# Kernel tuning notes

Measured on AMD Instinct MI355X. Metric: run time of the kernel, lower is better.

Reference implementation:

```python
import jax, jax.numpy as jnp
import numpy as np

B, S, D, H = 2, 2048, 1024, 16
DK = D // H

def setup_inputs() -> dict:
    key = jax.random.key(0)
    ks = jax.random.split(key, 12)
    def lin(k, shape, fan_in):
        bound = 1.0 / np.sqrt(fan_in)
        return jax.random.uniform(k, shape, jnp.float32, -bound, bound)
    inp = {
        'Q': jax.random.normal(ks[0], (B, S, D), jnp.float32),
        'K': jax.random.normal(ks[1], (B, S, D), jnp.float32),
        'V': jax.random.normal(ks[2], (B, S, D), jnp.float32),
        # padding mask: last 128 key positions of batch element 0 are padding
        'padding_mask': jnp.ones((B, 1, 1, S), jnp.int32).at[0, :, :, -128:].set(0),
        # causal look-ahead mask
        'look_ahead_mask': jnp.tril(jnp.ones((S, S), jnp.int32))[None, None],
        'Wq': lin(ks[3], (D, D), D), 'bq': lin(ks[4], (D,), D),
        'Wk': lin(ks[5], (D, D), D), 'bk': lin(ks[6], (D,), D),
        'Wv': lin(ks[7], (D, D), D), 'bv': lin(ks[8], (D,), D),
        'Wo': lin(ks[9], (D, D), D), 'bo': lin(ks[10], (D,), D),
    }
    return inp

def _split_heads(x):
    # [B,S,D] -> [B,H,S,DK]
    b, s, _ = x.shape
    return x.reshape(b, s, H, DK).transpose(0, 2, 1, 3)

def reference(Q, K, V, padding_mask, look_ahead_mask, Wq, bq, Wk, bk, Wv, bv, Wo, bo):
    q = _split_heads(Q @ Wq.T + bq)  # [B,H,S,DK]
    k = _split_heads(K @ Wk.T + bk)
    v = _split_heads(V @ Wv.T + bv)
    scores = jnp.einsum('bhqd,bhkd->bhqk', q, k) / np.sqrt(DK).astype(np.float32)
    neg_inf = jnp.float32(-jnp.inf)
    scores = jnp.where(padding_mask == 0, neg_inf, scores)
    scores = jnp.where(look_ahead_mask == 0, neg_inf, scores)
    weights = jax.nn.softmax(scores, axis=-1)  # dropout is identity in eval mode
    x = jnp.einsum('bhqk,bhkd->bhqd', weights, v)  # [B,H,S,DK]
    x = x.transpose(0, 2, 1, 3).reshape(Q.shape[0], Q.shape[1], D)
    return x @ Wo.T + bo
```

## Files before the change

kernel.cpp:

```cpp
#include <hip/hip_runtime.h>
#include <hip/hip_bf16.h>

#define B_   2
#define S_   2048
#define D_   1024
#define H_   16
#define DK_  64

typedef unsigned short u16;
typedef __attribute__((ext_vector_type(8))) short bf16x8;
typedef __attribute__((ext_vector_type(4))) float f32x4;

#define CHUNK_   12
#define NSLOT_   48

static __device__ __forceinline__ u16 f2bf(float f) {
  union { float f; unsigned u; } v; v.f = f;
  unsigned r = v.u + 0x7FFF + ((v.u >> 16) & 1);
  return (u16)(r >> 16);
}

static __device__ __forceinline__ void gl_lds16(const void* g, void* l) {
  __builtin_amdgcn_global_load_lds(
      (const __attribute__((address_space(1))) void*)g,
      (__attribute__((address_space(3))) void*)l, 16, 0, 0);
}

__global__ void cvt7(const float4* __restrict__ i0, const float4* __restrict__ i1,
                     const float4* __restrict__ i2, const float4* __restrict__ i3,
                     const float4* __restrict__ i4, const float4* __restrict__ i5,
                     const float4* __restrict__ i6,
                     ushort4* __restrict__ o0, ushort4* __restrict__ o1,
                     ushort4* __restrict__ o2, ushort4* __restrict__ o3,
                     ushort4* __restrict__ o4, ushort4* __restrict__ o5,
                     ushort4* __restrict__ o6, int nbig, int nsmall) {
  int y = blockIdx.y;
  const float4* in; ushort4* out; int bound;
  switch (y) {
    case 0: in = i0; out = o0; bound = nbig; break;
    case 1: in = i1; out = o1; bound = nbig; break;
    case 2: in = i2; out = o2; bound = nbig; break;
    case 3: in = i3; out = o3; bound = nsmall; break;
    case 4: in = i4; out = o4; bound = nsmall; break;
    case 5: in = i5; out = o5; bound = nsmall; break;
    default: in = i6; out = o6; bound = nsmall; break;
  }
  int i = blockIdx.x * blockDim.x + threadIdx.x;
  if (i < bound) {
    float4 v = in[i];
    ushort4 r;
    r.x = f2bf(v.x); r.y = f2bf(v.y); r.z = f2bf(v.z); r.w = f2bf(v.w);
    out[i] = r;
  }
}

__launch_bounds__(256, 3)
__global__ void gemm_qkv(const u16* __restrict__ Xq, const u16* __restrict__ Xk, const u16* __restrict__ Xv,
                         const u16* __restrict__ Wq, const u16* __restrict__ Wk, const u16* __restrict__ Wv,
                         const float* __restrict__ bq, const float* __restrict__ bk, const float* __restrict__ bv,
                         u16* __restrict__ outq, u16* __restrict__ outk, u16* __restrict__ outv) {
  const int z = blockIdx.z;
  const int lid = (int)blockIdx.x + 8 * (int)blockIdx.y;
  const int bx = (lid >> 3) & 7;
  const int by = (lid & 7) * 4 + (lid >> 6);

  const u16* Am; const u16* Bm; int m0, n0;
  if (z == 2) { Am = Wv; Bm = Xv; m0 = bx * 128; n0 = by * 128; }
  else if (z == 1) { Am = Xk; Bm = Wk; m0 = by * 128; n0 = bx * 128; }
  else { Am = Xq; Bm = Wq; m0 = by * 128; n0 = bx * 128; }
  const float* bias = (z == 0) ? bq : (z == 1) ? bk : bv;

  __shared__ __align__(16) u16 As[2][128 * 32];
  __shared__ __align__(16) u16 Bs[2][128 * 32];

  const int tid = threadIdx.x, lane = tid & 63, w = tid >> 6;
  const int q = lane >> 4, cl = lane & 15;
  const int wr = w >> 1, wc = w & 1;

  f32x4 acc[4][4] = {};

#pragma unroll
  for (int i = 0; i < 2; ++i) {
    int cb = (i * 4 + w) * 64;
    int ch = cb + lane;
    int row = ch >> 2, ko = (ch & 3) << 3;
    gl_lds16(Am + (size_t)(m0 + row) * D_ + ko, As[0] + cb * 8);
    gl_lds16(Bm + (size_t)(n0 + row) * D_ + ko, Bs[0] + cb * 8);
  }
  __syncthreads();

  int cur = 0;
  for (int k0 = 0; k0 < D_; k0 += 32) {
    if (k0 + 32 < D_) {
#pragma unroll
      for (int i = 0; i < 2; ++i) {
        int cb = (i * 4 + w) * 64;
        int ch = cb + lane;
        int row = ch >> 2, ko = (ch & 3) << 3;
        gl_lds16(Am + (size_t)(m0 + row) * D_ + k0 + 32 + ko, As[cur ^ 1] + cb * 8);
        gl_lds16(Bm + (size_t)(n0 + row) * D_ + k0 + 32 + ko, Bs[cur ^ 1] + cb * 8);
      }
    }

    const u16* Ac = As[cur];
    const u16* Bc = Bs[cur];
    bf16x8 af[4], bfr[4];
#pragma unroll
    for (int r = 0; r < 4; ++r) af[r]  = *(const bf16x8*)(Ac + (wr * 64 + r * 16 + cl) * 32 + q * 8);
#pragma unroll
    for (int c = 0; c < 4; ++c) bfr[c] = *(const bf16x8*)(Bc + (wc * 64 + c * 16 + cl) * 32 + q * 8);
#pragma unroll
    for (int r = 0; r < 4; ++r)
#pragma unroll
      for (int c = 0; c < 4; ++c)
        acc[r][c] = __builtin_amdgcn_mfma_f32_16x16x32_bf16(af[r], bfr[c], acc[r][c], 0, 0, 0);

    __syncthreads();
    cur ^= 1;
  }

  if (z == 2) {
#pragma unroll
    for (int r = 0; r < 4; ++r) {
#pragma unroll
      for (int rr = 0; rr < 4; ++rr) {
        int j = m0 + wr * 64 + r * 16 + q * 4 + rr;
        float bval = bias[j];
        int hh = j >> 6, dk = j & 63;
#pragma unroll
        for (int c = 0; c < 4; ++c) {
          int n = n0 + wc * 64 + c * 16 + cl;
          int bb = n >> 11, s = n & (S_ - 1);
          outv[((size_t)(bb * H_ + hh) * DK_ + dk) * S_ + s] = f2bf(acc[r][c][rr] + bval);
        }
      }
    }
  } else {
    const float scale = (z == 0) ? 0.125f : 1.0f;
    u16* o = (z == 0) ? outq : outk;
#pragma unroll
    for (int c = 0; c < 4; ++c) {
      int j = n0 + wc * 64 + c * 16 + cl;
      float bval = bias[j];
      int hh = j >> 6, dk = j & 63;
#pragma unroll
      for (int r = 0; r < 4; ++r) {
#pragma unroll
        for (int rr = 0; rr < 4; ++rr) {
          int n = m0 + wr * 64 + r * 16 + q * 4 + rr;
          int bb = n >> 11, s = n & (S_ - 1);
          o[((size_t)(bb * H_ + hh) * S_ + s) * DK_ + dk] = f2bf((acc[r][c][rr] + bval) * scale);
        }
      }
    }
  }
}

__launch_bounds__(256, 4)
__global__ void attn(const u16* __restrict__ qh, const u16* __restrict__ kh,
                     const u16* __restrict__ vt, const int* __restrict__ pad,
                     u16* __restrict__ attn_out, float* __restrict__ Po, float* __restrict__ Pl) {
  __shared__ __align__(16) u16 Ks[64 * 64];
  __shared__ __align__(16) u16 Vs[64 * 64];
  __shared__ __align__(16) u16 Ps[4][16 * 72];
  __shared__ float Kbias[64];

  const int tid = threadIdx.x, lane = tid & 63, w = tid >> 6;
  const int q = lane >> 4, cl = lane & 15;
  const int h = blockIdx.y, b = blockIdx.z;

  const int x = blockIdx.x;
  int qt, ch, nch;
  if (x < 24)      { qt = 24 + x / 3;          ch = x % 3;       nch = 3; }
  else if (x < 48) { int y = x - 24; qt = 12 + y / 2; ch = y & 1; nch = 2; }
  else             { qt = x - 48;              ch = 0;           nch = 1; }
  const int qb = qt * 64;
  const int t0 = ch * CHUNK_;
  const int t1 = (qt < t0 + CHUNK_ - 1) ? qt : (t0 + CHUNK_ - 1);

  const u16* Q = qh + (size_t)(b * H_ + h) * S_ * DK_;
  const u16* K = kh + (size_t)(b * H_ + h) * S_ * DK_;
  const u16* V = vt + (size_t)(b * H_ + h) * DK_ * S_;
  const int* pm = pad + b * S_;

  const int qr0 = qb + w * 16;
  bf16x8 qf0 = *(const bf16x8*)(Q + (qr0 + cl) * DK_ + q * 8);
  bf16x8 qf1 = *(const bf16x8*)(Q + (qr0 + cl) * DK_ + 32 + q * 8);

  f32x4 o[4] = {};
  float ls[4] = {0.f, 0.f, 0.f, 0.f};
  u16* Pw = Ps[w];

  for (int it = t0; it <= t1; ++it) {
    const int kb = it << 6;
#pragma unroll
    for (int i = 0; i < 2; ++i) {
      int s = (i * 4 + w) * 64 + lane;
      int row = s >> 3;
      int c = (s & 7) ^ (row & 7);
      gl_lds16(K + (size_t)(kb + row) * DK_ + (c << 3), Ks + (size_t)s * 8);
      gl_lds16(V + (size_t)row * S_ + kb + (c << 3), Vs + (size_t)s * 8);
    }
    if (tid < 64) {
      Kbias[tid] = (pm[kb + tid] != 0) ? -6.0f : -3e38f;
    }
    __syncthreads();

    f32x4 sa[4];
#pragma unroll
    for (int ct = 0; ct < 4; ++ct) {
      int rk = ct * 16 + cl;
      int c0 = q ^ (rk & 7);
      bf16x8 kf0 = *(const bf16x8*)(Ks + rk * 64 + (c0 << 3));
      bf16x8 kf1 = *(const bf16x8*)(Ks + rk * 64 + ((c0 ^ 4) << 3));
      f32x4 zz = {};
      zz = __builtin_amdgcn_mfma_f32_16x16x32_bf16(qf0, kf0, zz, 0, 0, 0);
      zz = __builtin_amdgcn_mfma_f32_16x16x32_bf16(qf1, kf1, zz, 0, 0, 0);
      sa[ct] = zz;
    }

    if (it < qt) {
#pragma unroll
      for (int ct = 0; ct < 4; ++ct) {
        float kbv = Kbias[ct * 16 + cl];
#pragma unroll
        for (int rr = 0; rr < 4; ++rr) {
          float p = __expf(sa[ct][rr] + kbv);
          ls[rr] += p;
          Pw[(q * 4 + rr) * 72 + ct * 16 + cl] = f2bf(p);
        }
      }
    } else {
#pragma unroll
      for (int ct = 0; ct < 4; ++ct) {
        int kg = kb + ct * 16 + cl;
        float kbv = Kbias[ct * 16 + cl];
#pragma unroll
        for (int rr = 0; rr < 4; ++rr) {
          int qg = qr0 + q * 4 + rr;
          float p = (kg <= qg) ? __expf(sa[ct][rr] + kbv) : 0.f;
          ls[rr] += p;
          Pw[(q * 4 + rr) * 72 + ct * 16 + cl] = f2bf(p);
        }
      }
    }

    bf16x8 pf0 = *(const bf16x8*)(Pw + cl * 72 + q * 8);
    bf16x8 pf1 = *(const bf16x8*)(Pw + cl * 72 + 32 + q * 8);

#pragma unroll
    for (int ct = 0; ct < 4; ++ct) {
      int rv = ct * 16 + cl;
      int c0 = q ^ (rv & 7);
      bf16x8 vf0 = *(const bf16x8*)(Vs + rv * 64 + (c0 << 3));
      bf16x8 vf1 = *(const bf16x8*)(Vs + rv * 64 + ((c0 ^ 4) << 3));
      o[ct] = __builtin_amdgcn_mfma_f32_16x16x32_bf16(pf0, vf0, o[ct], 0, 0, 0);
      o[ct] = __builtin_amdgcn_mfma_f32_16x16x32_bf16(pf1, vf1, o[ct], 0, 0, 0);
    }
    __syncthreads();
  }

  if (nch == 1) {
#pragma unroll
    for (int rr = 0; rr < 4; ++rr) {
      float l = ls[rr];
      l += __shfl_xor(l, 1, 64);
      l += __shfl_xor(l, 2, 64);
      l += __shfl_xor(l, 4, 64);
      l += __shfl_xor(l, 8, 64);
      float inv = 1.0f / l;
      int qg = qr0 + q * 4 + rr;
      size_t base = (size_t)(b * S_ + qg) * D_ + h * DK_;
#pragma unroll
      for (int ct = 0; ct < 4; ++ct)
        attn_out[base + ct * 16 + cl] = f2bf(o[ct][rr] * inv);
    }
  } else {
    int pq = qt - 12;
    int off = (pq < 12) ? pq * 2 : 24 + (pq - 12) * 3;
    size_t slot = (size_t)(b * H_ + h) * NSLOT_ + off + ch;
#pragma unroll
    for (int rr = 0; rr < 4; ++rr) {
      float l = ls[rr];
      l += __shfl_xor(l, 1, 64);
      l += __shfl_xor(l, 2, 64);
      l += __shfl_xor(l, 4, 64);
      l += __shfl_xor(l, 8, 64);
      int rl = w * 16 + q * 4 + rr;
      if (cl == 0) Pl[slot * 64 + rl] = l;
      float* po = Po + ((size_t)slot * 64 + rl) * 64;
#pragma unroll
      for (int ct = 0; ct < 4; ++ct)
        po[ct * 16 + cl] = o[ct][rr];
    }
  }
}

__global__ void combine(const float* __restrict__ Po, const float* __restrict__ Pl,
                        u16* __restrict__ attn_out) {
  const int x = blockIdx.x, h = blockIdx.y, b = blockIdx.z;
  const int qt = 12 + (x >> 4);
  const int inner = ((x & 15) << 8) + threadIdx.x;
  const int r = inner >> 6, c = inner & 63;

  const int nch = (qt < 24) ? 2 : 3;
  const int pq = qt - 12;
  const int off = (pq < 12) ? pq * 2 : 24 + (pq - 12) * 3;
  const size_t slot0 = (size_t)(b * H_ + h) * NSLOT_ + off;

  float os = 0.f, lsum = 0.f;
  for (int ch = 0; ch < nch; ++ch) {
    os += Po[((slot0 + ch) * 64 + r) * 64 + c];
    lsum += Pl[(slot0 + ch) * 64 + r];
  }
  int qg = qt * 64 + r;
  attn_out[(size_t)(b * S_ + qg) * D_ + h * DK_ + c] = f2bf(os / lsum);
}

__launch_bounds__(256, 2)
__global__ void gemm_out(const u16* __restrict__ A, const u16* __restrict__ W,
                         const float* __restrict__ bias, float* __restrict__ out) {
  __shared__ __align__(16) u16 As[2][64 * 32];
  __shared__ __align__(16) u16 Bs[2][128 * 32];

  const int tid = threadIdx.x, lane = tid & 63, w = tid >> 6;
  const int q = lane >> 4, cl = lane & 15;
  const int wr = w >> 1, wc = w & 1;
  const int lid = (int)blockIdx.x + 8 * (int)blockIdx.y;
  const int bx = (lid >> 3) & 7;
  const int by = (lid & 7) * 8 + (lid >> 6);
  const int m0 = by * 64, n0 = bx * 128;

  f32x4 acc[2][4] = {};

  {
    int cb = w * 64;
    int chA = cb + lane;
    int rowA = chA >> 2, koA = (chA & 3) << 3;
    gl_lds16(A + (size_t)(m0 + rowA) * D_ + koA, As[0] + cb * 8);
#pragma unroll
    for (int i = 0; i < 2; ++i) {
      int cbB = (i * 4 + w) * 64;
      int chB = cbB + lane;
      int rowB = chB >> 2, koB = (chB & 3) << 3;
      gl_lds16(W + (size_t)(n0 + rowB) * D_ + koB, Bs[0] + cbB * 8);
    }
  }
  __syncthreads();

  int cur = 0;
  for (int k0 = 0; k0 < D_; k0 += 32) {
    if (k0 + 32 < D_) {
      int cb = w * 64;
      int chA = cb + lane;
      int rowA = chA >> 2, koA = (chA & 3) << 3;
      gl_lds16(A + (size_t)(m0 + rowA) * D_ + k0 + 32 + koA, As[cur ^ 1] + cb * 8);
#pragma unroll
      for (int i = 0; i < 2; ++i) {
        int cbB = (i * 4 + w) * 64;
        int chB = cbB + lane;
        int rowB = chB >> 2, koB = (chB & 3) << 3;
        gl_lds16(W + (size_t)(n0 + rowB) * D_ + k0 + 32 + koB, Bs[cur ^ 1] + cbB * 8);
      }
    }

    const u16* Ac = As[cur];
    const u16* Bc = Bs[cur];
    bf16x8 af[2], bfr[4];
#pragma unroll
    for (int r = 0; r < 2; ++r) af[r]  = *(const bf16x8*)(Ac + (wr * 32 + r * 16 + cl) * 32 + q * 8);
#pragma unroll
    for (int c = 0; c < 4; ++c) bfr[c] = *(const bf16x8*)(Bc + (wc * 64 + c * 16 + cl) * 32 + q * 8);
#pragma unroll
    for (int r = 0; r < 2; ++r)
#pragma unroll
      for (int c = 0; c < 4; ++c)
        acc[r][c] = __builtin_amdgcn_mfma_f32_16x16x32_bf16(af[r], bfr[c], acc[r][c], 0, 0, 0);

    __syncthreads();
    cur ^= 1;
  }

#pragma unroll
  for (int c = 0; c < 4; ++c) {
    int j = n0 + wc * 64 + c * 16 + cl;
    float bval = bias[j];
#pragma unroll
    for (int r = 0; r < 2; ++r) {
#pragma unroll
      for (int rr = 0; rr < 4; ++rr) {
        int n = m0 + wr * 32 + r * 16 + q * 4 + rr;
        out[(size_t)n * D_ + j] = acc[r][c][rr] + bval;
      }
    }
  }
}

extern "C" void kernel_launch(void* const* d_in, const int* in_sizes, int n_in,
                              void* d_out, int out_size, void* d_ws, size_t ws_size,
                              hipStream_t stream) {
  const float* Qf  = (const float*)d_in[0];
  const float* Kf  = (const float*)d_in[1];
  const float* Vf  = (const float*)d_in[2];
  const int*   pad = (const int*)d_in[3];
  const float* Wqf = (const float*)d_in[5];
  const float* bq  = (const float*)d_in[6];
  const float* Wkf = (const float*)d_in[7];
  const float* bk  = (const float*)d_in[8];
  const float* Wvf = (const float*)d_in[9];
  const float* bv  = (const float*)d_in[10];
  const float* Wof = (const float*)d_in[11];
  const float* bo  = (const float*)d_in[12];

  const size_t BSD = (size_t)B_ * S_ * D_;
  const size_t DD  = (size_t)D_ * D_;

  char* ws = (char*)d_ws;
  u16* Qb   = (u16*)ws; ws += BSD * 2;
  u16* Kb   = (u16*)ws; ws += BSD * 2;
  u16* Vb   = (u16*)ws; ws += BSD * 2;
  u16* Wqb  = (u16*)ws; ws += DD * 2;
  u16* Wkb  = (u16*)ws; ws += DD * 2;
  u16* Wvb  = (u16*)ws; ws += DD * 2;
  u16* Wob  = (u16*)ws; ws += DD * 2;
  u16* qhd  = (u16*)ws; ws += BSD * 2;
  u16* khd  = (u16*)ws; ws += BSD * 2;
  u16* vtd  = (u16*)ws; ws += BSD * 2;
  u16* attn_o = (u16*)ws; ws += BSD * 2;

  float* Po = (float*)d_ws;
  float* Pl = Po + (size_t)B_ * H_ * NSLOT_ * 64 * 64;

  const int n4 = (int)(BSD / 4);
  const int w4 = (int)(DD / 4);
  dim3 gc(n4 / 256, 7);
  cvt7<<<gc, 256, 0, stream>>>((const float4*)Qf, (const float4*)Kf, (const float4*)Vf,
                               (const float4*)Wqf, (const float4*)Wkf, (const float4*)Wvf, (const float4*)Wof,
                               (ushort4*)Qb, (ushort4*)Kb, (ushort4*)Vb,
                               (ushort4*)Wqb, (ushort4*)Wkb, (ushort4*)Wvb, (ushort4*)Wob, n4, w4);

  dim3 g1(D_ / 128, (B_ * S_) / 128, 3);
  gemm_qkv<<<g1, 256, 0, stream>>>(Qb, Kb, Vb, Wqb, Wkb, Wvb, bq, bk, bv, qhd, khd, vtd);

  dim3 g2(60, H_, B_);
  attn<<<g2, 256, 0, stream>>>(qhd, khd, vtd, pad, attn_o, Po, Pl);

  dim3 g2b(320, H_, B_);
  combine<<<g2b, 256, 0, stream>>>(Po, Pl, attn_o);

  dim3 g3(D_ / 128, (B_ * S_) / 64);
  gemm_out<<<g3, 256, 0, stream>>>(attn_o, Wob, bo, (float*)d_out);
}
```

Before: 245.6 us.

## Fuse split-KV partial combine into output projection A-tile staging

Removes the separate combine kernel and instead reduces the split-chunk partial outputs and normalizers inside gemm_out while staging the A tile into LDS for query tiles that were split. This saves one kernel launch and the bf16 round trip of the combined attention output. In exchange, each of the 8 column blocks recomputes the same combine reads, and the fused path uses synchronous register loads and stores instead of async global-to-LDS copies, which may stall the double-buffer pipeline.

```diff
diff --git a/kernel.cpp b/kernel.cpp
--- a/kernel.cpp
+++ b/kernel.cpp
@@ -296,30 +296,10 @@
   }
 }
 
-__global__ void combine(const float* __restrict__ Po, const float* __restrict__ Pl,
-                        u16* __restrict__ attn_out) {
-  const int x = blockIdx.x, h = blockIdx.y, b = blockIdx.z;
-  const int qt = 12 + (x >> 4);
-  const int inner = ((x & 15) << 8) + threadIdx.x;
-  const int r = inner >> 6, c = inner & 63;
-
-  const int nch = (qt < 24) ? 2 : 3;
-  const int pq = qt - 12;
-  const int off = (pq < 12) ? pq * 2 : 24 + (pq - 12) * 3;
-  const size_t slot0 = (size_t)(b * H_ + h) * NSLOT_ + off;
-
-  float os = 0.f, lsum = 0.f;
-  for (int ch = 0; ch < nch; ++ch) {
-    os += Po[((slot0 + ch) * 64 + r) * 64 + c];
-    lsum += Pl[(slot0 + ch) * 64 + r];
-  }
-  int qg = qt * 64 + r;
-  attn_out[(size_t)(b * S_ + qg) * D_ + h * DK_ + c] = f2bf(os / lsum);
-}
-
 __launch_bounds__(256, 2)
 __global__ void gemm_out(const u16* __restrict__ A, const u16* __restrict__ W,
-                         const float* __restrict__ bias, float* __restrict__ out) {
+                         const float* __restrict__ bias, float* __restrict__ out,
+                         const float* __restrict__ Po, const float* __restrict__ Pl) {
   __shared__ __align__(16) u16 As[2][64 * 32];
   __shared__ __align__(16) u16 Bs[2][128 * 32];
 
@@ -331,13 +311,49 @@
   const int by = (lid & 7) * 8 + (lid >> 6);
   const int m0 = by * 64, n0 = bx * 128;
 
+  const int bb = m0 >> 11;
+  const int qt = (m0 & (S_ - 1)) >> 6;
+  const bool fused = (qt >= 12);
+  int nch = 0, off = 0;
+  if (fused) {
+    int pq = qt - 12;
+    off = (pq < 12) ? pq * 2 : 24 + (pq - 12) * 3;
+    nch = (qt < 24) ? 2 : 3;
+  }
+
+  const int chA = w * 64 + lane;
+  const int rowA = chA >> 2, koA = (chA & 3) << 3;
+
   f32x4 acc[2][4] = {};
 
+  auto stage_a = [&](u16* dst, int kk0) {
+    if (!fused) {
+      gl_lds16(A + (size_t)(m0 + rowA) * D_ + kk0 + koA, dst + chA * 8);
+    } else {
+      const int hh = kk0 >> 6, dk0 = kk0 & 63;
+      const size_t slot0 = (size_t)(bb * H_ + hh) * NSLOT_ + off;
+      float s0 = 0.f, s1 = 0.f, s2 = 0.f, s3 = 0.f, s4 = 0.f, s5 = 0.f, s6 = 0.f, s7 = 0.f;
+      float lsum = 0.f;
+      for (int cc = 0; cc < nch; ++cc) {
+        const float* po = Po + (((slot0 + cc) * 64 + rowA) * 64 + dk0 + koA);
+        float4 u0 = *(const float4*)po;
+        float4 u1 = *(const float4*)(po + 4);
+        s0 += u0.x; s1 += u0.y; s2 += u0.z; s3 += u0.w;
+        s4 += u1.x; s5 += u1.y; s6 += u1.z; s7 += u1.w;
+        lsum += Pl[(slot0 + cc) * 64 + rowA];
+      }
+      float inv = 1.0f / lsum;
+      bf16x8 pk;
+      pk[0] = (short)f2bf(s0 * inv); pk[1] = (short)f2bf(s1 * inv);
+      pk[2] = (short)f2bf(s2 * inv); pk[3] = (short)f2bf(s3 * inv);
+      pk[4] = (short)f2bf(s4 * inv); pk[5] = (short)f2bf(s5 * inv);
+      pk[6] = (short)f2bf(s6 * inv); pk[7] = (short)f2bf(s7 * inv);
+      *(bf16x8*)(dst + chA * 8) = pk;
+    }
+  };
+
   {
-    int cb = w * 64;
-    int chA = cb + lane;
-    int rowA = chA >> 2, koA = (chA & 3) << 3;
-    gl_lds16(A + (size_t)(m0 + rowA) * D_ + koA, As[0] + cb * 8);
+    stage_a(As[0], 0);
 #pragma unroll
     for (int i = 0; i < 2; ++i) {
       int cbB = (i * 4 + w) * 64;
@@ -351,10 +367,7 @@
   int cur = 0;
   for (int k0 = 0; k0 < D_; k0 += 32) {
     if (k0 + 32 < D_) {
-      int cb = w * 64;
-      int chA = cb + lane;
-      int rowA = chA >> 2, koA = (chA & 3) << 3;
-      gl_lds16(A + (size_t)(m0 + rowA) * D_ + k0 + 32 + koA, As[cur ^ 1] + cb * 8);
+      stage_a(As[cur ^ 1], k0 + 32);
 #pragma unroll
       for (int i = 0; i < 2; ++i) {
         int cbB = (i * 4 + w) * 64;
@@ -445,9 +458,6 @@
   dim3 g2(60, H_, B_);
   attn<<<g2, 256, 0, stream>>>(qhd, khd, vtd, pad, attn_o, Po, Pl);
 
-  dim3 g2b(320, H_, B_);
-  combine<<<g2b, 256, 0, stream>>>(Po, Pl, attn_o);
-
   dim3 g3(D_ / 128, (B_ * S_) / 64);
-  gemm_out<<<g3, 256, 0, stream>>>(attn_o, Wob, bo, (float*)d_out);
-}
+  gemm_out<<<g3, 256, 0, stream>>>(attn_o, Wob, bo, (float*)d_out, Po, Pl);
+}
```

After: 267.0 us. +8.7%, slower.

## Enlarge attention query tile to 128 rows for K/V reuse

Applied to the files above, without the earlier changes.

Each attention block now covers 128 query rows instead of 64, and every wave handles two 16-row groups. Each K/V tile staged in LDS is therefore reused for twice as many queries, halving global K/V traffic and sync count per query. The split-KV chunking, slot layout and combine indexing are redone to match. In exchange there are half as many blocks, higher register and LDS pressure per block (launch bound lowered to 3), and more wasted work on fully masked diagonal tiles.

```diff
diff --git a/kernel.cpp b/kernel.cpp
--- a/kernel.cpp
+++ b/kernel.cpp
@@ -11,8 +11,7 @@
 typedef __attribute__((ext_vector_type(8))) short bf16x8;
 typedef __attribute__((ext_vector_type(4))) float f32x4;
 
-#define CHUNK_   12
-#define NSLOT_   48
+#define NSLOT_   24
 
 static __device__ __forceinline__ u16 f2bf(float f) {
   union { float f; unsigned u; } v; v.f = f;
@@ -156,13 +155,13 @@
   }
 }
 
-__launch_bounds__(256, 4)
+__launch_bounds__(256, 3)
 __global__ void attn(const u16* __restrict__ qh, const u16* __restrict__ kh,
                      const u16* __restrict__ vt, const int* __restrict__ pad,
                      u16* __restrict__ attn_out, float* __restrict__ Po, float* __restrict__ Pl) {
   __shared__ __align__(16) u16 Ks[64 * 64];
   __shared__ __align__(16) u16 Vs[64 * 64];
-  __shared__ __align__(16) u16 Ps[4][16 * 72];
+  __shared__ __align__(16) u16 Ps[4][32 * 72];
   __shared__ float Kbias[64];
 
   const int tid = threadIdx.x, lane = tid & 63, w = tid >> 6;
@@ -171,24 +170,29 @@
 
   const int x = blockIdx.x;
   int qt, ch, nch;
-  if (x < 24)      { qt = 24 + x / 3;          ch = x % 3;       nch = 3; }
-  else if (x < 48) { int y = x - 24; qt = 12 + y / 2; ch = y & 1; nch = 2; }
-  else             { qt = x - 48;              ch = 0;           nch = 1; }
-  const int qb = qt * 64;
-  const int t0 = ch * CHUNK_;
-  const int t1 = (qt < t0 + CHUNK_ - 1) ? qt : (t0 + CHUNK_ - 1);
+  if (x < 12)      { qt = 12 + x / 3;          ch = x % 3;       nch = 3; }
+  else if (x < 24) { int y = x - 12; qt = 6 + y / 2; ch = y & 1; nch = 2; }
+  else             { qt = x - 24;              ch = 0;           nch = 1; }
+  const int qb = qt * 128;
+  const int nkv = 2 * qt + 2;
+  const int t0 = ch * nkv / nch;
+  const int t1 = (ch + 1) * nkv / nch - 1;
 
   const u16* Q = qh + (size_t)(b * H_ + h) * S_ * DK_;
   const u16* K = kh + (size_t)(b * H_ + h) * S_ * DK_;
   const u16* V = vt + (size_t)(b * H_ + h) * DK_ * S_;
   const int* pm = pad + b * S_;
 
-  const int qr0 = qb + w * 16;
-  bf16x8 qf0 = *(const bf16x8*)(Q + (qr0 + cl) * DK_ + q * 8);
-  bf16x8 qf1 = *(const bf16x8*)(Q + (qr0 + cl) * DK_ + 32 + q * 8);
-
-  f32x4 o[4] = {};
-  float ls[4] = {0.f, 0.f, 0.f, 0.f};
+  const int qr0 = qb + w * 32;
+  bf16x8 qf[2][2];
+#pragma unroll
+  for (int rg = 0; rg < 2; ++rg) {
+    qf[rg][0] = *(const bf16x8*)(Q + (qr0 + rg * 16 + cl) * DK_ + q * 8);
+    qf[rg][1] = *(const bf16x8*)(Q + (qr0 + rg * 16 + cl) * DK_ + 32 + q * 8);
+  }
+
+  f32x4 o[2][4] = {};
+  float ls[2][4] = {};
   u16* Pw = Ps[w];
 
   for (int it = t0; it <= t1; ++it) {
@@ -206,92 +210,104 @@
     }
     __syncthreads();
 
-    f32x4 sa[4];
-#pragma unroll
-    for (int ct = 0; ct < 4; ++ct) {
-      int rk = ct * 16 + cl;
-      int c0 = q ^ (rk & 7);
-      bf16x8 kf0 = *(const bf16x8*)(Ks + rk * 64 + (c0 << 3));
-      bf16x8 kf1 = *(const bf16x8*)(Ks + rk * 64 + ((c0 ^ 4) << 3));
-      f32x4 zz = {};
-      zz = __builtin_amdgcn_mfma_f32_16x16x32_bf16(qf0, kf0, zz, 0, 0, 0);
-      zz = __builtin_amdgcn_mfma_f32_16x16x32_bf16(qf1, kf1, zz, 0, 0, 0);
-      sa[ct] = zz;
-    }
-
-    if (it < qt) {
+    const bool masked = (kb >= qb);
+
+#pragma unroll
+    for (int rg = 0; rg < 2; ++rg) {
+      const int qrg = qr0 + rg * 16;
+
+      f32x4 sa[4];
 #pragma unroll
       for (int ct = 0; ct < 4; ++ct) {
-        float kbv = Kbias[ct * 16 + cl];
-#pragma unroll
-        for (int rr = 0; rr < 4; ++rr) {
-          float p = __expf(sa[ct][rr] + kbv);
-          ls[rr] += p;
-          Pw[(q * 4 + rr) * 72 + ct * 16 + cl] = f2bf(p);
+        int rk = ct * 16 + cl;
+        int c0 = q ^ (rk & 7);
+        bf16x8 kf0 = *(const bf16x8*)(Ks + rk * 64 + (c0 << 3));
+        bf16x8 kf1 = *(const bf16x8*)(Ks + rk * 64 + ((c0 ^ 4) << 3));
+        f32x4 zz = {};
+        zz = __builtin_amdgcn_mfma_f32_16x16x32_bf16(qf[rg][0], kf0, zz, 0, 0, 0);
+        zz = __builtin_amdgcn_mfma_f32_16x16x32_bf16(qf[rg][1], kf1, zz, 0, 0, 0);
+        sa[ct] = zz;
+      }
+
+      if (!masked) {
+#pragma unroll
+        for (int ct = 0; ct < 4; ++ct) {
+          float kbv = Kbias[ct * 16 + cl];
+#pragma unroll
+          for (int rr = 0; rr < 4; ++rr) {
+            float p = __expf(sa[ct][rr] + kbv);
+            ls[rg][rr] += p;
+            Pw[(rg * 16 + q * 4 + rr) * 72 + ct * 16 + cl] = f2bf(p);
+          }
         }
-      }
-    } else {
+      } else {
+#pragma unroll
+        for (int ct = 0; ct < 4; ++ct) {
+          int kg = kb + ct * 16 + cl;
+          float kbv = Kbias[ct * 16 + cl];
+#pragma unroll
+          for (int rr = 0; rr < 4; ++rr) {
+            int qg = qrg + q * 4 + rr;
+            float p = (kg <= qg) ? __expf(sa[ct][rr] + kbv) : 0.f;
+            ls[rg][rr] += p;
+            Pw[(rg * 16 + q * 4 + rr) * 72 + ct * 16 + cl] = f2bf(p);
+          }
+        }
+      }
+
+      bf16x8 pf0 = *(const bf16x8*)(Pw + (rg * 16 + cl) * 72 + q * 8);
+      bf16x8 pf1 = *(const bf16x8*)(Pw + (rg * 16 + cl) * 72 + 32 + q * 8);
+
 #pragma unroll
       for (int ct = 0; ct < 4; ++ct) {
-        int kg = kb + ct * 16 + cl;
-        float kbv = Kbias[ct * 16 + cl];
-#pragma unroll
-        for (int rr = 0; rr < 4; ++rr) {
-          int qg = qr0 + q * 4 + rr;
-          float p = (kg <= qg) ? __expf(sa[ct][rr] + kbv) : 0.f;
-          ls[rr] += p;
-          Pw[(q * 4 + rr) * 72 + ct * 16 + cl] = f2bf(p);
-        }
-      }
-    }
-
-    bf16x8 pf0 = *(const bf16x8*)(Pw + cl * 72 + q * 8);
-    bf16x8 pf1 = *(const bf16x8*)(Pw + cl * 72 + 32 + q * 8);
-
-#pragma unroll
-    for (int ct = 0; ct < 4; ++ct) {
-      int rv = ct * 16 + cl;
-      int c0 = q ^ (rv & 7);
-      bf16x8 vf0 = *(const bf16x8*)(Vs + rv * 64 + (c0 << 3));
-      bf16x8 vf1 = *(const bf16x8*)(Vs + rv * 64 + ((c0 ^ 4) << 3));
-      o[ct] = __builtin_amdgcn_mfma_f32_16x16x32_bf16(pf0, vf0, o[ct], 0, 0, 0);
-      o[ct] = __builtin_amdgcn_mfma_f32_16x16x32_bf16(pf1, vf1, o[ct], 0, 0, 0);
+        int rv = ct * 16 + cl;
+        int c0 = q ^ (rv & 7);
+        bf16x8 vf0 = *(const bf16x8*)(Vs + rv * 64 + (c0 << 3));
+        bf16x8 vf1 = *(const bf16x8*)(Vs + rv * 64 + ((c0 ^ 4) << 3));
+        o[rg][ct] = __builtin_amdgcn_mfma_f32_16x16x32_bf16(pf0, vf0, o[rg][ct], 0, 0, 0);
+        o[rg][ct] = __builtin_amdgcn_mfma_f32_16x16x32_bf16(pf1, vf1, o[rg][ct], 0, 0, 0);
+      }
     }
     __syncthreads();
   }
 
   if (nch == 1) {
 #pragma unroll
-    for (int rr = 0; rr < 4; ++rr) {
-      float l = ls[rr];
-      l += __shfl_xor(l, 1, 64);
-      l += __shfl_xor(l, 2, 64);
-      l += __shfl_xor(l, 4, 64);
-      l += __shfl_xor(l, 8, 64);
-      float inv = 1.0f / l;
-      int qg = qr0 + q * 4 + rr;
-      size_t base = (size_t)(b * S_ + qg) * D_ + h * DK_;
-#pragma unroll
-      for (int ct = 0; ct < 4; ++ct)
-        attn_out[base + ct * 16 + cl] = f2bf(o[ct][rr] * inv);
+    for (int rg = 0; rg < 2; ++rg) {
+#pragma unroll
+      for (int rr = 0; rr < 4; ++rr) {
+        float l = ls[rg][rr];
+        l += __shfl_xor(l, 1, 64);
+        l += __shfl_xor(l, 2, 64);
+        l += __shfl_xor(l, 4, 64);
+        l += __shfl_xor(l, 8, 64);
+        float inv = 1.0f / l;
+        int qg = qr0 + rg * 16 + q * 4 + rr;
+        size_t base = (size_t)(b * S_ + qg) * D_ + h * DK_;
+#pragma unroll
+        for (int ct = 0; ct < 4; ++ct)
+          attn_out[base + ct * 16 + cl] = f2bf(o[rg][ct][rr] * inv);
+      }
     }
   } else {
-    int pq = qt - 12;
-    int off = (pq < 12) ? pq * 2 : 24 + (pq - 12) * 3;
+    int off = (qt < 12) ? (qt - 6) * 2 : 12 + (qt - 12) * 3;
     size_t slot = (size_t)(b * H_ + h) * NSLOT_ + off + ch;
 #pragma unroll
-    for (int rr = 0; rr < 4; ++rr) {
-      float l = ls[rr];
-      l += __shfl_xor(l, 1, 64);
-      l += __shfl_xor(l, 2, 64);
-      l += __shfl_xor(l, 4, 64);
-      l += __shfl_xor(l, 8, 64);
-      int rl = w * 16 + q * 4 + rr;
-      if (cl == 0) Pl[slot * 64 + rl] = l;
-      float* po = Po + ((size_t)slot * 64 + rl) * 64;
-#pragma unroll
-      for (int ct = 0; ct < 4; ++ct)
-        po[ct * 16 + cl] = o[ct][rr];
+    for (int rg = 0; rg < 2; ++rg) {
+#pragma unroll
+      for (int rr = 0; rr < 4; ++rr) {
+        float l = ls[rg][rr];
+        l += __shfl_xor(l, 1, 64);
+        l += __shfl_xor(l, 2, 64);
+        l += __shfl_xor(l, 4, 64);
+        l += __shfl_xor(l, 8, 64);
+        int rl = w * 32 + rg * 16 + q * 4 + rr;
+        if (cl == 0) Pl[slot * 128 + rl] = l;
+        float* po = Po + ((size_t)slot * 128 + rl) * 64;
+#pragma unroll
+        for (int ct = 0; ct < 4; ++ct)
+          po[ct * 16 + cl] = o[rg][ct][rr];
+      }
     }
   }
 }
@@ -299,21 +315,20 @@
 __global__ void combine(const float* __restrict__ Po, const float* __restrict__ Pl,
                         u16* __restrict__ attn_out) {
   const int x = blockIdx.x, h = blockIdx.y, b = blockIdx.z;
-  const int qt = 12 + (x >> 4);
-  const int inner = ((x & 15) << 8) + threadIdx.x;
+  const int qt = 6 + (x >> 5);
+  const int inner = ((x & 31) << 8) + threadIdx.x;
   const int r = inner >> 6, c = inner & 63;
 
-  const int nch = (qt < 24) ? 2 : 3;
-  const int pq = qt - 12;
-  const int off = (pq < 12) ? pq * 2 : 24 + (pq - 12) * 3;
+  const int nch = (qt < 12) ? 2 : 3;
+  const int off = (qt < 12) ? (qt - 6) * 2 : 12 + (qt - 12) * 3;
   const size_t slot0 = (size_t)(b * H_ + h) * NSLOT_ + off;
 
   float os = 0.f, lsum = 0.f;
   for (int ch = 0; ch < nch; ++ch) {
-    os += Po[((slot0 + ch) * 64 + r) * 64 + c];
-    lsum += Pl[(slot0 + ch) * 64 + r];
-  }
-  int qg = qt * 64 + r;
+    os += Po[((slot0 + ch) * 128 + r) * 64 + c];
+    lsum += Pl[(slot0 + ch) * 128 + r];
+  }
+  int qg = qt * 128 + r;
   attn_out[(size_t)(b * S_ + qg) * D_ + h * DK_ + c] = f2bf(os / lsum);
 }
 
@@ -429,7 +444,7 @@
   u16* attn_o = (u16*)ws; ws += BSD * 2;
 
   float* Po = (float*)d_ws;
-  float* Pl = Po + (size_t)B_ * H_ * NSLOT_ * 64 * 64;
+  float* Pl = Po + (size_t)B_ * H_ * NSLOT_ * 128 * 64;
 
   const int n4 = (int)(BSD / 4);
   const int w4 = (int)(DD / 4);
@@ -442,7 +457,7 @@
   dim3 g1(D_ / 128, (B_ * S_) / 128, 3);
   gemm_qkv<<<g1, 256, 0, stream>>>(Qb, Kb, Vb, Wqb, Wkb, Wvb, bq, bk, bv, qhd, khd, vtd);
 
-  dim3 g2(60, H_, B_);
+  dim3 g2(30, H_, B_);
   attn<<<g2, 256, 0, stream>>>(qhd, khd, vtd, pad, attn_o, Po, Pl);
 
   dim3 g2b(320, H_, B_);
```

After: 253.3 us. 3.1% more time.
